# Kernel optimization log

Measured on AMD Instinct MI355X. Metric: run time of the kernel, lower is better.

The kernel has to match this reference:

```python
import jax, jax.numpy as jnp
import numpy as np

N = 100000
DIM = 128
E_A = 500000
E_D = 500000


def setup_inputs() -> dict:
    key = jax.random.key(0)
    ks = jax.random.split(key, 8)
    h = jax.random.normal(ks[0], (N, DIM), dtype=jnp.float32)
    a_idx = jax.random.randint(ks[1], (E_A, 3), 0, N, dtype=jnp.int64 if jax.config.jax_enable_x64 else jnp.int32)
    a_val = jax.random.uniform(ks[2], (E_A, 1), dtype=jnp.float32)
    d_idx = jax.random.randint(ks[3], (E_D, 4), 0, N, dtype=jnp.int64 if jax.config.jax_enable_x64 else jnp.int32)
    d_val = jax.random.uniform(ks[4], (E_D, 1), dtype=jnp.float32)
    # Linear weights stored as [in, out]; init ~ Kaiming-uniform-ish scale
    W_a = jax.random.normal(ks[5], (3 * DIM + 1, DIM), dtype=jnp.float32) * (1.0 / np.sqrt(3 * DIM + 1))
    b_a = jnp.zeros((DIM,), dtype=jnp.float32)
    W_d = jax.random.normal(ks[6], (4 * DIM + 1, DIM), dtype=jnp.float32) * (1.0 / np.sqrt(4 * DIM + 1))
    b_d = jnp.zeros((DIM,), dtype=jnp.float32)
    W_h = jax.random.normal(ks[7], (3 * DIM, DIM), dtype=jnp.float32) * (1.0 / np.sqrt(3 * DIM))
    b_h = jnp.zeros((DIM,), dtype=jnp.float32)
    return {"h": h, "a_idx": a_idx, "a_val": a_val, "d_idx": d_idx, "d_val": d_val,
            "W_a": W_a, "b_a": b_a, "W_d": W_d, "b_d": b_d, "W_h": W_h, "b_h": b_h}


def reference(h, a_idx, a_val, d_idx, d_val, W_a, b_a, W_d, b_d, W_h, b_h):
    n = h.shape[0]
    # angle messages: gather 3 node embeddings + scalar, Linear + SiLU, scatter to center node
    x_a = jnp.concatenate([h[a_idx[:, 0]], h[a_idx[:, 1]], h[a_idx[:, 2]], a_val], axis=-1)  # [E_a, 3d+1]
    m_ijk = jax.nn.silu(x_a @ W_a + b_a)  # [E_a, d]
    agg_a = jax.ops.segment_sum(m_ijk, a_idx[:, 1], num_segments=n)  # [N, d]
    # dihedral messages: gather 4 node embeddings + scalar
    x_d = jnp.concatenate([h[d_idx[:, 0]], h[d_idx[:, 1]], h[d_idx[:, 2]], h[d_idx[:, 3]], d_val], axis=-1)  # [E_d, 4d+1]
    m_ijkl = jax.nn.silu(x_d @ W_d + b_d)  # [E_d, d]
    agg_d = jax.ops.segment_sum(m_ijkl, d_idx[:, 1], num_segments=n)  # [N, d]
    # residual node update
    return h + jnp.concatenate([h, agg_a, agg_d], axis=-1) @ W_h + b_h
```

## Files before the change

kernel.cpp:

```cpp
#include <hip/hip_runtime.h>
#include <hip/hip_bf16.h>

#define DIM 128
#define LDS_STRIDE 136
#define SC_STRIDE 132

typedef __attribute__((ext_vector_type(8))) __bf16 bf16x8;
typedef __attribute__((ext_vector_type(4))) __bf16 bf16x4;
typedef __attribute__((ext_vector_type(4))) float f32x4;

__global__ __launch_bounds__(256) void prep_w(const float* __restrict__ W_a,
                                              const float* __restrict__ W_d,
                                              const float* __restrict__ W_h,
                                              __bf16* __restrict__ Wt)
{
    int idx = blockIdx.x * 256 + threadIdx.x;
    if (idx >= 10 * 16384) return;
    int t   = idx >> 14;
    int rem = idx & 16383;
    int c   = rem >> 7;
    int k   = rem & 127;
    const float* src;
    if (t < 4)      src = W_d + (size_t)t * 16384;
    else if (t < 7) src = W_a + (size_t)(t - 4) * 16384;
    else            src = W_h + (size_t)(t - 7) * 16384;
    Wt[(size_t)t * 16384 + c * 128 + k] = (__bf16)src[k * 128 + c];
}

__global__ __launch_bounds__(256) void h2bf(const float* __restrict__ h,
                                            __bf16* __restrict__ hb, int n)
{
    int i = (blockIdx.x * 256 + threadIdx.x) * 8;
    if (i >= n) return;
    float4 v0 = *(const float4*)(h + i);
    float4 v1 = *(const float4*)(h + i + 4);
    bf16x8 o;
    o[0] = (__bf16)v0.x; o[1] = (__bf16)v0.y; o[2] = (__bf16)v0.z; o[3] = (__bf16)v0.w;
    o[4] = (__bf16)v1.x; o[5] = (__bf16)v1.y; o[6] = (__bf16)v1.z; o[7] = (__bf16)v1.w;
    *(bf16x8*)(hb + i) = o;
}

__device__ __forceinline__ void stage_wt(const __bf16* __restrict__ Wtj,
                                         __bf16 (*sB)[LDS_STRIDE], int tid)
{
    for (int it = 0; it < 8; ++it) {
        int idx = tid + it * 256;
        int c  = idx >> 4;
        int k8 = (idx & 15) << 3;
        *(bf16x8*)&sB[c][k8] = *(const bf16x8*)(Wtj + c * 128 + k8);
    }
}

__device__ __forceinline__ void load_afrag_f32(const float* __restrict__ src,
                                               int row, int lk, int N, bf16x8 afrag[4])
{
    const float* rp = src + (size_t)row * DIM;
    #pragma unroll
    for (int ks = 0; ks < 4; ++ks) {
        float4 v0 = make_float4(0.f, 0.f, 0.f, 0.f), v1 = v0;
        if (row < N) {
            v0 = *(const float4*)(rp + ks * 32 + lk);
            v1 = *(const float4*)(rp + ks * 32 + lk + 4);
        }
        bf16x8 a;
        a[0] = (__bf16)v0.x; a[1] = (__bf16)v0.y; a[2] = (__bf16)v0.z; a[3] = (__bf16)v0.w;
        a[4] = (__bf16)v1.x; a[5] = (__bf16)v1.y; a[6] = (__bf16)v1.z; a[7] = (__bf16)v1.w;
        afrag[ks] = a;
    }
}

__device__ __forceinline__ void load_afrag_bf16(const __bf16* __restrict__ src,
                                                int row, int lk, int N, bf16x8 afrag[4])
{
    const __bf16* rp = src + (size_t)row * DIM;
    #pragma unroll
    for (int ks = 0; ks < 4; ++ks) {
        bf16x8 a = {};
        if (row < N) a = *(const bf16x8*)(rp + ks * 32 + lk);
        afrag[ks] = a;
    }
}

__global__ __launch_bounds__(256, 4) void proj(const __bf16* __restrict__ src,
                                               const __bf16* __restrict__ Wt,
                                               __bf16* __restrict__ dst,
                                               int N)
{
    __shared__ __bf16 sB[128][LDS_STRIDE];
    float* sC = reinterpret_cast<float*>(sB);
    const int tid = threadIdx.x;
    const int j = blockIdx.y;
    const int node0 = blockIdx.x * 64;
    const int wave = tid >> 6, lane = tid & 63;
    const int lrow = lane & 15;
    const int lk   = (lane >> 4) * 8;
    const int arow = node0 + wave * 16 + lrow;

    stage_wt(Wt + (size_t)j * 16384, sB, tid);

    bf16x8 afrag[4];
    load_afrag_bf16(src, arow, lk, N, afrag);
    __syncthreads();

    f32x4 acc[8];
    #pragma unroll
    for (int ct = 0; ct < 8; ++ct) acc[ct] = (f32x4){0.f, 0.f, 0.f, 0.f};

    #pragma unroll
    for (int ks = 0; ks < 4; ++ks) {
        int k0 = ks * 32 + lk;
        #pragma unroll
        for (int ct = 0; ct < 8; ++ct) {
            bf16x8 b = *(const bf16x8*)&sB[ct * 16 + lrow][k0];
            acc[ct] = __builtin_amdgcn_mfma_f32_16x16x32_bf16(afrag[ks], b, acc[ct], 0, 0, 0);
        }
    }

    __syncthreads();
    {
        int rbase = wave * 16 + (lane >> 4) * 4;
        #pragma unroll
        for (int r = 0; r < 4; ++r)
            #pragma unroll
            for (int ct = 0; ct < 8; ++ct)
                sC[(rbase + r) * SC_STRIDE + ct * 16 + lrow] = acc[ct][r];
    }
    __syncthreads();

    __bf16* dj = dst + (size_t)j * N * DIM;
    for (int it = 0; it < 8; ++it) {
        int idx = tid + it * 256;
        int row = idx >> 5;
        int c4  = (idx & 31) << 2;
        int grow = node0 + row;
        if (grow < N) {
            const float* sp = sC + row * SC_STRIDE + c4;
            bf16x4 o;
            o[0] = (__bf16)sp[0]; o[1] = (__bf16)sp[1];
            o[2] = (__bf16)sp[2]; o[3] = (__bf16)sp[3];
            *(bf16x4*)(dj + (size_t)grow * DIM + c4) = o;
        }
    }
}

__global__ __launch_bounds__(256) void csr_count_both(const int* __restrict__ a_idx,
                                                      const int* __restrict__ d_idx,
                                                      int* __restrict__ offs,
                                                      int EA, int ED, int N)
{
    int e = blockIdx.x * 256 + threadIdx.x;
    if (e < EA) {
        atomicAdd(&offs[a_idx[3 * (size_t)e + 1]], 1);
    } else if (e < EA + ED) {
        int k = e - EA;
        atomicAdd(&offs[N + d_idx[4 * (size_t)k + 1]], 1);
    }
}

#define SCAN_CHUNK 1024

__global__ __launch_bounds__(256) void scan_s1(int* __restrict__ data,
                                               int* __restrict__ partials, int n)
{
    __shared__ int lds[256];
    const int t = threadIdx.x;
    const int base = blockIdx.x * SCAN_CHUNK + t * 4;
    int v[4];
    #pragma unroll
    for (int i = 0; i < 4; ++i) v[i] = (base + i < n) ? data[base + i] : 0;
    int tsum = v[0] + v[1] + v[2] + v[3];
    lds[t] = tsum; __syncthreads();
    for (int off = 1; off < 256; off <<= 1) {
        int x = (t >= off) ? lds[t - off] : 0;
        __syncthreads();
        lds[t] += x;
        __syncthreads();
    }
    if (t == 255) partials[blockIdx.x] = lds[255];
    int run = lds[t] - tsum;
    #pragma unroll
    for (int i = 0; i < 4; ++i) {
        int nv = run; run += v[i];
        if (base + i < n) data[base + i] = nv;
    }
}

__global__ __launch_bounds__(256) void scan_s2(int* __restrict__ partials, int nb)
{
    __shared__ int lds[256];
    const int t = threadIdx.x;
    int v = (t < nb) ? partials[t] : 0;
    lds[t] = v; __syncthreads();
    for (int off = 1; off < 256; off <<= 1) {
        int x = (t >= off) ? lds[t - off] : 0;
        __syncthreads();
        lds[t] += x;
        __syncthreads();
    }
    if (t < nb) partials[t] = lds[t] - v;
}

__global__ __launch_bounds__(256) void scan_s3(int* __restrict__ data,
                                               const int* __restrict__ partials, int n)
{
    const int add = partials[blockIdx.x];
    const int base = blockIdx.x * SCAN_CHUNK + threadIdx.x * 4;
    #pragma unroll
    for (int i = 0; i < 4; ++i)
        if (base + i < n) data[base + i] += add;
}

__global__ __launch_bounds__(256) void csr_fill_both(const int* __restrict__ a_idx,
                                                     const float* __restrict__ a_val,
                                                     const int* __restrict__ d_idx,
                                                     const float* __restrict__ d_val,
                                                     int* __restrict__ offs,
                                                     int4* __restrict__ recs,
                                                     int EA, int ED, int N)
{
    int e = blockIdx.x * 256 + threadIdx.x;
    if (e < EA) {
        int i0 = a_idx[3 * (size_t)e + 0];
        int i1 = a_idx[3 * (size_t)e + 1];
        int i2 = a_idx[3 * (size_t)e + 2];
        int slot = atomicAdd(&offs[i1], 1);
        recs[slot] = make_int4(i0 * 256, i2 * 256, __float_as_int(a_val[e]), 0);
    } else if (e < EA + ED) {
        int k = e - EA;
        int i0 = d_idx[4 * (size_t)k + 0];
        int i1 = d_idx[4 * (size_t)k + 1];
        int i2 = d_idx[4 * (size_t)k + 2];
        int i3 = d_idx[4 * (size_t)k + 3];
        int slot = atomicAdd(&offs[N + i1], 1);
        recs[slot] = make_int4(i0 * 256, i2 * 256, i3 * 256, __float_as_int(d_val[k]));
    }
}

__device__ __forceinline__ float silu(float x) { return x / (1.f + __expf(-x)); }

__global__ __launch_bounds__(256) void gather3(const __bf16* __restrict__ P,
                                               const float* __restrict__ wlast,
                                               const float* __restrict__ bias,
                                               const int* __restrict__ offs,
                                               const int4* __restrict__ recs,
                                               float* __restrict__ aggf, int N)
{
    const int tid = threadIdx.x;
    const int n = blockIdx.x * 4 + (tid >> 6);
    if (n >= N) return;
    const int lane = tid & 63;
    const int half = lane >> 5;
    const int gl = lane & 31;
    const int f  = gl * 4;
    const int fb = gl * 8;
    const size_t NBb = (size_t)N * DIM * 2;
    const char* P0b = (const char*)P;
    const char* P1b = P0b + NBb;
    const char* P2b = P0b + 2 * NBb;
    int start = (n == 0) ? 0 : offs[n - 1];
    int end = offs[n];

    float wl[4], base[4];
    {
        const float* wp = wlast + f;
        const float* bp = bias + f;
        bf16x4 p1 = *(const bf16x4*)(P1b + (size_t)n * 256 + fb);
        #pragma unroll
        for (int c = 0; c < 4; ++c) { wl[c] = wp[c]; base[c] = (float)p1[c] + bp[c]; }
    }
    float a[4] = {0.f, 0.f, 0.f, 0.f};

    const int cnt = end - start;
    const int npair = cnt >> 1;
    int s = start;
    for (int p = 0; p < npair; ++p, s += 2) {
        int4 r = recs[s + half];
        bf16x4 q0 = *(const bf16x4*)(P0b + r.x + fb);
        bf16x4 q2 = *(const bf16x4*)(P2b + r.y + fb);
        float v = __int_as_float(r.z);
        #pragma unroll
        for (int c = 0; c < 4; ++c)
            a[c] += silu((float)q0[c] + (float)q2[c] + v * wl[c] + base[c]);
    }
    if (cnt & 1) {
        int4 r = recs[end - 1];
        bf16x4 q0 = *(const bf16x4*)(P0b + r.x + fb);
        bf16x4 q2 = *(const bf16x4*)(P2b + r.y + fb);
        float v = __int_as_float(r.z);
        if (half == 0) {
            #pragma unroll
            for (int c = 0; c < 4; ++c)
                a[c] += silu((float)q0[c] + (float)q2[c] + v * wl[c] + base[c]);
        }
    }
    #pragma unroll
    for (int c = 0; c < 4; ++c) a[c] += __shfl_xor(a[c], 32, 64);
    if (half == 0) {
        f32x4 o;
        #pragma unroll
        for (int c = 0; c < 4; ++c) o[c] = a[c];
        *(f32x4*)(aggf + (size_t)n * DIM + f) = o;
    }
}

__global__ __launch_bounds__(256) void gather4(const __bf16* __restrict__ P,
                                               const float* __restrict__ wlast,
                                               const float* __restrict__ bias,
                                               const int* __restrict__ offs_d,
                                               const int4* __restrict__ recs,
                                               __bf16* __restrict__ agg, int N)
{
    const int tid = threadIdx.x;
    const int n = blockIdx.x * 4 + (tid >> 6);
    if (n >= N) return;
    const int lane = tid & 63;
    const int half = lane >> 5;
    const int gl = lane & 31;
    const int f  = gl * 4;
    const int fb = gl * 8;
    const size_t NBb = (size_t)N * DIM * 2;
    const char* P0b = (const char*)P;
    const char* P1b = P0b + NBb;
    const char* P2b = P0b + 2 * NBb;
    const char* P3b = P0b + 3 * NBb;
    int start = offs_d[n - 1];
    int end = offs_d[n];

    float wl[4], base[4];
    {
        const float* wp = wlast + f;
        const float* bp = bias + f;
        bf16x4 p1 = *(const bf16x4*)(P1b + (size_t)n * 256 + fb);
        #pragma unroll
        for (int c = 0; c < 4; ++c) { wl[c] = wp[c]; base[c] = (float)p1[c] + bp[c]; }
    }
    float a[4] = {0.f, 0.f, 0.f, 0.f};

    const int cnt = end - start;
    const int npair = cnt >> 1;
    int s = start;
    for (int p = 0; p < npair; ++p, s += 2) {
        int4 r = recs[s + half];
        bf16x4 q0 = *(const bf16x4*)(P0b + r.x + fb);
        bf16x4 q2 = *(const bf16x4*)(P2b + r.y + fb);
        bf16x4 q3 = *(const bf16x4*)(P3b + r.z + fb);
        float v = __int_as_float(r.w);
        #pragma unroll
        for (int c = 0; c < 4; ++c)
            a[c] += silu((float)q0[c] + (float)q2[c] + (float)q3[c] + v * wl[c] + base[c]);
    }
    if (cnt & 1) {
        int4 r = recs[end - 1];
        bf16x4 q0 = *(const bf16x4*)(P0b + r.x + fb);
        bf16x4 q2 = *(const bf16x4*)(P2b + r.y + fb);
        bf16x4 q3 = *(const bf16x4*)(P3b + r.z + fb);
        float v = __int_as_float(r.w);
        if (half == 0) {
            #pragma unroll
            for (int c = 0; c < 4; ++c)
                a[c] += silu((float)q0[c] + (float)q2[c] + (float)q3[c] + v * wl[c] + base[c]);
        }
    }
    #pragma unroll
    for (int c = 0; c < 4; ++c) a[c] += __shfl_xor(a[c], 32, 64);
    if (half == 0) {
        bf16x4 o;
        #pragma unroll
        for (int c = 0; c < 4; ++c) o[c] = (__bf16)a[c];
        *(bf16x4*)(agg + (size_t)n * DIM + f) = o;
    }
}

__global__ __launch_bounds__(256, 4) void update2(const float* __restrict__ h,
                                                  const float* __restrict__ aggA,
                                                  const __bf16* __restrict__ aggD,
                                                  const __bf16* __restrict__ PH,
                                                  const __bf16* __restrict__ Wt,
                                                  const float* __restrict__ bh,
                                                  float* __restrict__ out, int N)
{
    __shared__ __bf16 sB[128][LDS_STRIDE];
    float* sC = reinterpret_cast<float*>(sB);
    const int tid = threadIdx.x;
    const int node0 = blockIdx.x * 64;
    const int wave = tid >> 6, lane = tid & 63;
    const int lrow = lane & 15;
    const int lk   = (lane >> 4) * 8;
    const int arow = node0 + wave * 16 + lrow;

    bf16x8 aA[4], aD[4];
    load_afrag_f32(aggA, arow, lk, N, aA);
    load_afrag_bf16(aggD, arow, lk, N, aD);

    f32x4 acc[8];
    #pragma unroll
    for (int ct = 0; ct < 8; ++ct) acc[ct] = (f32x4){0.f, 0.f, 0.f, 0.f};

    #pragma unroll
    for (int s = 0; s < 2; ++s) {
        __syncthreads();
        stage_wt(Wt + (size_t)s * 16384, sB, tid);
        __syncthreads();

        #pragma unroll
        for (int ks = 0; ks < 4; ++ks) {
            int k0 = ks * 32 + lk;
            #pragma unroll
            for (int ct = 0; ct < 8; ++ct) {
                bf16x8 b = *(const bf16x8*)&sB[ct * 16 + lrow][k0];
                bf16x8 af = (s == 0) ? aA[ks] : aD[ks];
                acc[ct] = __builtin_amdgcn_mfma_f32_16x16x32_bf16(af, b, acc[ct], 0, 0, 0);
            }
        }
    }

    __syncthreads();
    {
        int rbase = wave * 16 + (lane >> 4) * 4;
        #pragma unroll
        for (int r = 0; r < 4; ++r)
            #pragma unroll
            for (int ct = 0; ct < 8; ++ct)
                sC[(rbase + r) * SC_STRIDE + ct * 16 + lrow] = acc[ct][r];
    }
    __syncthreads();

    for (int it = 0; it < 8; ++it) {
        int idx = tid + it * 256;
        int row = idx >> 5;
        int c4  = (idx & 31) << 2;
        int grow = node0 + row;
        if (grow < N) {
            const float* sp = sC + row * SC_STRIDE + c4;
            float4 rv = *(const float4*)(h + (size_t)grow * DIM + c4);
            float4 bv = *(const float4*)(bh + c4);
            bf16x4 pv = *(const bf16x4*)(PH + (size_t)grow * DIM + c4);
            float4 ov;
            ov.x = rv.x + bv.x + (float)pv[0] + sp[0];
            ov.y = rv.y + bv.y + (float)pv[1] + sp[1];
            ov.z = rv.z + bv.z + (float)pv[2] + sp[2];
            ov.w = rv.w + bv.w + (float)pv[3] + sp[3];
            *(float4*)(out + (size_t)grow * DIM + c4) = ov;
        }
    }
}

static inline size_t align16(size_t x) { return (x + 15) & ~(size_t)15; }

extern "C" void kernel_launch(void* const* d_in, const int* in_sizes, int n_in,
                              void* d_out, int out_size, void* d_ws, size_t ws_size,
                              hipStream_t stream)
{
    const float* h     = (const float*)d_in[0];
    const int*   a_idx = (const int*)d_in[1];
    const float* a_val = (const float*)d_in[2];
    const int*   d_idx = (const int*)d_in[3];
    const float* d_val = (const float*)d_in[4];
    const float* W_a   = (const float*)d_in[5];
    const float* b_a   = (const float*)d_in[6];
    const float* W_d   = (const float*)d_in[7];
    const float* b_d   = (const float*)d_in[8];
    const float* W_h   = (const float*)d_in[9];
    const float* b_h   = (const float*)d_in[10];
    float* out = (float*)d_out;

    const int N  = in_sizes[0] / DIM;
    const int EA = in_sizes[2];
    const int ED = in_sizes[4];
    const size_t NB = (size_t)N * DIM;
    const int twoN = 2 * N;
    const int NBLK = (twoN + SCAN_CHUNK - 1) / SCAN_CHUNK;

    size_t off = 0;
    __bf16* P    = (__bf16*)((char*)d_ws + off); off = align16(off + 4 * NB * sizeof(__bf16));
    __bf16* aggD = (__bf16*)((char*)d_ws + off); off = align16(off + NB * sizeof(__bf16));
    int* offs     = (int*)((char*)d_ws + off);  off = align16(off + (size_t)twoN * sizeof(int));
    int* partials = (int*)((char*)d_ws + off);  off = align16(off + 256 * sizeof(int));
    int4* recs    = (int4*)((char*)d_ws + off); off = align16(off + (size_t)(EA + ED) * sizeof(int4));
    __bf16* Wt  = (__bf16*)((char*)d_ws + off); off = align16(off + (size_t)10 * 16384 * sizeof(__bf16));
    if (ws_size < off) return;

    const int NT64 = (N + 63) / 64;
    const int GE = (EA + ED + 255) / 256;
    const int GN4 = (N + 3) / 4;

    __bf16* h_bf = (__bf16*)d_out;

    prep_w<<<(10 * 16384 + 255) / 256, 256, 0, stream>>>(W_a, W_d, W_h, Wt);
    h2bf<<<(int)(NB / 8 + 255) / 256, 256, 0, stream>>>(h, h_bf, (int)NB);

    hipMemsetAsync(offs, 0, (size_t)twoN * sizeof(int), stream);
    csr_count_both<<<GE, 256, 0, stream>>>(a_idx, d_idx, offs, EA, ED, N);
    scan_s1<<<NBLK, 256, 0, stream>>>(offs, partials, twoN);
    scan_s2<<<1, 256, 0, stream>>>(partials, NBLK);
    scan_s3<<<NBLK, 256, 0, stream>>>(offs, partials, twoN);
    csr_fill_both<<<GE, 256, 0, stream>>>(a_idx, a_val, d_idx, d_val, offs, recs, EA, ED, N);

    {
        dim3 g(NT64, 4);
        proj<<<g, 256, 0, stream>>>(h_bf, Wt, P, N);
    }
    gather4<<<GN4, 256, 0, stream>>>(P, W_d + 512 * DIM, b_d, offs + N, recs, aggD, N);

    {
        dim3 g(NT64, 4);
        proj<<<g, 256, 0, stream>>>(h_bf, Wt + (size_t)4 * 16384, P, N);
    }
    gather3<<<GN4, 256, 0, stream>>>(P, W_a + 384 * DIM, b_a, offs, recs, out, N);

    update2<<<NT64, 256, 0, stream>>>(h, out, aggD, P + 3 * NB, Wt + (size_t)8 * 16384,
                                      b_h, out, N);
}
```

Measured before the change: 354.6 us.

## Merge prep kernels with CSR count and fuse CSR fill with dihedral projection

Folds the weight transpose, the h-to-bf16 conversion and the CSR count into one launch that partitions work by block index. It also merges the CSR fill pass with the first projection GEMM, so independent memory-bound scatter work and MFMA work share one grid. Projection grids become 1D with the tile and matrix index interleaved. This removes several launches and the idle tail between them. The fill blocks now also carry the projection kernel's LDS allocation and launch bounds, which may lower their occupancy.

```diff
diff --git a/kernel.cpp b/kernel.cpp
--- a/kernel.cpp
+++ b/kernel.cpp
@@ -9,35 +9,55 @@
 typedef __attribute__((ext_vector_type(4))) __bf16 bf16x4;
 typedef __attribute__((ext_vector_type(4))) float f32x4;
 
-__global__ __launch_bounds__(256) void prep_w(const float* __restrict__ W_a,
-                                              const float* __restrict__ W_d,
-                                              const float* __restrict__ W_h,
-                                              __bf16* __restrict__ Wt)
-{
-    int idx = blockIdx.x * 256 + threadIdx.x;
-    if (idx >= 10 * 16384) return;
-    int t   = idx >> 14;
-    int rem = idx & 16383;
-    int c   = rem >> 7;
-    int k   = rem & 127;
-    const float* src;
-    if (t < 4)      src = W_d + (size_t)t * 16384;
-    else if (t < 7) src = W_a + (size_t)(t - 4) * 16384;
-    else            src = W_h + (size_t)(t - 7) * 16384;
-    Wt[(size_t)t * 16384 + c * 128 + k] = (__bf16)src[k * 128 + c];
-}
-
-__global__ __launch_bounds__(256) void h2bf(const float* __restrict__ h,
-                                            __bf16* __restrict__ hb, int n)
-{
-    int i = (blockIdx.x * 256 + threadIdx.x) * 8;
-    if (i >= n) return;
-    float4 v0 = *(const float4*)(h + i);
-    float4 v1 = *(const float4*)(h + i + 4);
-    bf16x8 o;
-    o[0] = (__bf16)v0.x; o[1] = (__bf16)v0.y; o[2] = (__bf16)v0.z; o[3] = (__bf16)v0.w;
-    o[4] = (__bf16)v1.x; o[5] = (__bf16)v1.y; o[6] = (__bf16)v1.z; o[7] = (__bf16)v1.w;
-    *(bf16x8*)(hb + i) = o;
+
+__global__ __launch_bounds__(256) void count_prep(const int* __restrict__ a_idx,
+                                                  const int* __restrict__ d_idx,
+                                                  int* __restrict__ offs,
+                                                  const float* __restrict__ h,
+                                                  __bf16* __restrict__ hb,
+                                                  const float* __restrict__ W_a,
+                                                  const float* __restrict__ W_d,
+                                                  const float* __restrict__ W_h,
+                                                  __bf16* __restrict__ Wt,
+                                                  int EA, int ED, int N,
+                                                  int GE, int HB)
+{
+    const int b = blockIdx.x;
+    const int tid = threadIdx.x;
+    if (b < GE) {
+        int e = b * 256 + tid;
+        if (e < EA) {
+            atomicAdd(&offs[a_idx[3 * (size_t)e + 1]], 1);
+        } else if (e < EA + ED) {
+            int k = e - EA;
+            atomicAdd(&offs[N + d_idx[4 * (size_t)k + 1]], 1);
+        }
+        return;
+    }
+    if (b < GE + HB) {
+        int i = ((b - GE) * 256 + tid) * 8;
+        if (i >= N * DIM) return;
+        float4 v0 = *(const float4*)(h + i);
+        float4 v1 = *(const float4*)(h + i + 4);
+        bf16x8 o;
+        o[0] = (__bf16)v0.x; o[1] = (__bf16)v0.y; o[2] = (__bf16)v0.z; o[3] = (__bf16)v0.w;
+        o[4] = (__bf16)v1.x; o[5] = (__bf16)v1.y; o[6] = (__bf16)v1.z; o[7] = (__bf16)v1.w;
+        *(bf16x8*)(hb + i) = o;
+        return;
+    }
+    {
+        int idx = (b - GE - HB) * 256 + tid;
+        if (idx >= 10 * 16384) return;
+        int t   = idx >> 14;
+        int rem = idx & 16383;
+        int c   = rem >> 7;
+        int k   = rem & 127;
+        const float* src;
+        if (t < 4)      src = W_d + (size_t)t * 16384;
+        else if (t < 7) src = W_a + (size_t)(t - 4) * 16384;
+        else            src = W_h + (size_t)(t - 7) * 16384;
+        Wt[(size_t)t * 16384 + c * 128 + k] = (__bf16)src[k * 128 + c];
+    }
 }
 
 __device__ __forceinline__ void stage_wt(const __bf16* __restrict__ Wtj,
@@ -81,23 +101,19 @@
     }
 }
 
-__global__ __launch_bounds__(256, 4) void proj(const __bf16* __restrict__ src,
-                                               const __bf16* __restrict__ Wt,
-                                               __bf16* __restrict__ dst,
-                                               int N)
-{
-    __shared__ __bf16 sB[128][LDS_STRIDE];
+__device__ __forceinline__ void proj_body(const __bf16* __restrict__ src,
+                                          const __bf16* __restrict__ Wtj,
+                                          __bf16* __restrict__ dj,
+                                          __bf16 (*sB)[LDS_STRIDE],
+                                          int node0, int tid, int N)
+{
     float* sC = reinterpret_cast<float*>(sB);
-    const int tid = threadIdx.x;
-    const int j = blockIdx.y;
-    const int node0 = blockIdx.x * 64;
     const int wave = tid >> 6, lane = tid & 63;
     const int lrow = lane & 15;
     const int lk   = (lane >> 4) * 8;
     const int arow = node0 + wave * 16 + lrow;
 
-    stage_wt(Wt + (size_t)j * 16384, sB, tid);
-
+    stage_wt(Wtj, sB, tid);
     bf16x8 afrag[4];
     load_afrag_bf16(src, arow, lk, N, afrag);
     __syncthreads();
@@ -127,7 +143,6 @@
     }
     __syncthreads();
 
-    __bf16* dj = dst + (size_t)j * N * DIM;
     for (int it = 0; it < 8; ++it) {
         int idx = tid + it * 256;
         int row = idx >> 5;
@@ -143,18 +158,54 @@
     }
 }
 
-__global__ __launch_bounds__(256) void csr_count_both(const int* __restrict__ a_idx,
-                                                      const int* __restrict__ d_idx,
-                                                      int* __restrict__ offs,
-                                                      int EA, int ED, int N)
-{
-    int e = blockIdx.x * 256 + threadIdx.x;
-    if (e < EA) {
-        atomicAdd(&offs[a_idx[3 * (size_t)e + 1]], 1);
-    } else if (e < EA + ED) {
-        int k = e - EA;
-        atomicAdd(&offs[N + d_idx[4 * (size_t)k + 1]], 1);
-    }
+__global__ __launch_bounds__(256, 4) void fill_projD(const int* __restrict__ a_idx,
+                                                     const float* __restrict__ a_val,
+                                                     const int* __restrict__ d_idx,
+                                                     const float* __restrict__ d_val,
+                                                     int* __restrict__ offs,
+                                                     int4* __restrict__ recs,
+                                                     const __bf16* __restrict__ hb,
+                                                     const __bf16* __restrict__ Wt,
+                                                     __bf16* __restrict__ P,
+                                                     int EA, int ED, int N, int FILLB)
+{
+    __shared__ __bf16 sB[128][LDS_STRIDE];
+    const int tid = threadIdx.x;
+    if ((int)blockIdx.x < FILLB) {
+        int e = blockIdx.x * 256 + tid;
+        if (e < EA) {
+            int i0 = a_idx[3 * (size_t)e + 0];
+            int i1 = a_idx[3 * (size_t)e + 1];
+            int i2 = a_idx[3 * (size_t)e + 2];
+            int slot = atomicAdd(&offs[i1], 1);
+            recs[slot] = make_int4(i0 * 256, i2 * 256, __float_as_int(a_val[e]), 0);
+        } else if (e < EA + ED) {
+            int k = e - EA;
+            int i0 = d_idx[4 * (size_t)k + 0];
+            int i1 = d_idx[4 * (size_t)k + 1];
+            int i2 = d_idx[4 * (size_t)k + 2];
+            int i3 = d_idx[4 * (size_t)k + 3];
+            int slot = atomicAdd(&offs[N + i1], 1);
+            recs[slot] = make_int4(i0 * 256, i2 * 256, i3 * 256, __float_as_int(d_val[k]));
+        }
+        return;
+    }
+    int pb = blockIdx.x - FILLB;
+    int tile = pb >> 2, j = pb & 3;
+    proj_body(hb, Wt + (size_t)j * 16384, P + (size_t)j * N * DIM,
+              sB, tile * 64, tid, N);
+}
+
+__global__ __launch_bounds__(256, 4) void proj(const __bf16* __restrict__ src,
+                                               const __bf16* __restrict__ Wt,
+                                               __bf16* __restrict__ dst,
+                                               int N)
+{
+    __shared__ __bf16 sB[128][LDS_STRIDE];
+    const int pb = blockIdx.x;
+    const int tile = pb >> 2, j = pb & 3;
+    proj_body(src, Wt + (size_t)j * 16384, dst + (size_t)j * N * DIM,
+              sB, tile * 64, threadIdx.x, N);
 }
 
 #define SCAN_CHUNK 1024
@@ -208,32 +259,6 @@
     #pragma unroll
     for (int i = 0; i < 4; ++i)
         if (base + i < n) data[base + i] += add;
-}
-
-__global__ __launch_bounds__(256) void csr_fill_both(const int* __restrict__ a_idx,
-                                                     const float* __restrict__ a_val,
-                                                     const int* __restrict__ d_idx,
-                                                     const float* __restrict__ d_val,
-                                                     int* __restrict__ offs,
-                                                     int4* __restrict__ recs,
-                                                     int EA, int ED, int N)
-{
-    int e = blockIdx.x * 256 + threadIdx.x;
-    if (e < EA) {
-        int i0 = a_idx[3 * (size_t)e + 0];
-        int i1 = a_idx[3 * (size_t)e + 1];
-        int i2 = a_idx[3 * (size_t)e + 2];
-        int slot = atomicAdd(&offs[i1], 1);
-        recs[slot] = make_int4(i0 * 256, i2 * 256, __float_as_int(a_val[e]), 0);
-    } else if (e < EA + ED) {
-        int k = e - EA;
-        int i0 = d_idx[4 * (size_t)k + 0];
-        int i1 = d_idx[4 * (size_t)k + 1];
-        int i2 = d_idx[4 * (size_t)k + 2];
-        int i3 = d_idx[4 * (size_t)k + 3];
-        int slot = atomicAdd(&offs[N + i1], 1);
-        recs[slot] = make_int4(i0 * 256, i2 * 256, i3 * 256, __float_as_int(d_val[k]));
-    }
 }
 
 __device__ __forceinline__ float silu(float x) { return x / (1.f + __expf(-x)); }
@@ -482,30 +507,29 @@
 
     const int NT64 = (N + 63) / 64;
     const int GE = (EA + ED + 255) / 256;
+    const int HB = (int)((NB / 8 + 255) / 256);
+    const int WB = (10 * 16384 + 255) / 256;
     const int GN4 = (N + 3) / 4;
 
     __bf16* h_bf = (__bf16*)d_out;
 
-    prep_w<<<(10 * 16384 + 255) / 256, 256, 0, stream>>>(W_a, W_d, W_h, Wt);
-    h2bf<<<(int)(NB / 8 + 255) / 256, 256, 0, stream>>>(h, h_bf, (int)NB);
-
     hipMemsetAsync(offs, 0, (size_t)twoN * sizeof(int), stream);
-    csr_count_both<<<GE, 256, 0, stream>>>(a_idx, d_idx, offs, EA, ED, N);
+    count_prep<<<GE + HB + WB, 256, 0, stream>>>(a_idx, d_idx, offs, h, h_bf,
+                                                 W_a, W_d, W_h, Wt,
+                                                 EA, ED, N, GE, HB);
+
     scan_s1<<<NBLK, 256, 0, stream>>>(offs, partials, twoN);
     scan_s2<<<1, 256, 0, stream>>>(partials, NBLK);
     scan_s3<<<NBLK, 256, 0, stream>>>(offs, partials, twoN);
-    csr_fill_both<<<GE, 256, 0, stream>>>(a_idx, a_val, d_idx, d_val, offs, recs, EA, ED, N);
-
-    {
-        dim3 g(NT64, 4);
-        proj<<<g, 256, 0, stream>>>(h_bf, Wt, P, N);
-    }
+
+    fill_projD<<<GE + NT64 * 4, 256, 0, stream>>>(a_idx, a_val, d_idx, d_val,
+                                                  offs, recs, h_bf, Wt, P,
+                                                  EA, ED, N, GE);
+
     gather4<<<GN4, 256, 0, stream>>>(P, W_d + 512 * DIM, b_d, offs + N, recs, aggD, N);
 
-    {
-        dim3 g(NT64, 4);
-        proj<<<g, 256, 0, stream>>>(h_bf, Wt + (size_t)4 * 16384, P, N);
-    }
+    proj<<<NT64 * 4, 256, 0, stream>>>(h_bf, Wt + (size_t)4 * 16384, P, N);
+
     gather3<<<GN4, 256, 0, stream>>>(P, W_a + 384 * DIM, b_a, offs, recs, out, N);
 
     update2<<<NT64, 256, 0, stream>>>(h, out, aggD, P + 3 * NB, Wt + (size_t)8 * 16384,
```

Result: no change. 360.5 us (+1.7%).
